# Performance work log

Hardware: AMD Instinct MI355X
Metric: run time of the kernel (lower is better)

The kernel has to match this reference:

```python
import jax, jax.numpy as jnp
import numpy as np
import math

DIM = 64
N_, H_, W_ = 8, 64, 64
EPS = 1e-5


def setup_inputs() -> dict:
    key = jax.random.key(0)
    ks = jax.random.split(key, 11)
    c = DIM
    s = 1.0 / math.sqrt(c)
    x = jax.random.normal(ks[0], (N_, c, H_, W_), dtype=jnp.float32)
    return {
        "x": x,
        "gamma": jnp.ones((c,), jnp.float32),
        "beta": jnp.zeros((c,), jnp.float32),
        "wq": jax.random.normal(ks[1], (c, c), jnp.float32) * s,
        "bq": jax.random.normal(ks[2], (c,), jnp.float32) * 0.01,
        "wk": jax.random.normal(ks[3], (c, c), jnp.float32) * s,
        "bk": jax.random.normal(ks[4], (c,), jnp.float32) * 0.01,
        "wv": jax.random.normal(ks[5], (c, c), jnp.float32) * s,
        "bv": jax.random.normal(ks[6], (c,), jnp.float32) * 0.01,
        "wo": jax.random.normal(ks[7], (c, c), jnp.float32) * s,
        "bo": jax.random.normal(ks[8], (c,), jnp.float32) * 0.01,
    }


def _conv1x1(x, w, b):
    # 1x1 conv == channel mixing: x [n,c,h,w], w [out,in], b [out]
    return jnp.einsum('nchw,oc->nohw', x, w) + b[None, :, None, None]


def _batchnorm(x, gamma, beta):
    # training-mode BatchNorm2d: biased batch stats over (N,H,W)
    mean = jnp.mean(x, axis=(0, 2, 3), keepdims=True)
    var = jnp.var(x, axis=(0, 2, 3), keepdims=True)
    xn = (x - mean) * jax.lax.rsqrt(var + EPS)
    return xn * gamma[None, :, None, None] + beta[None, :, None, None]


def reference(x, gamma, beta, wq, bq, wk, bk, wv, bv, wo, bo):
    n, c, h, w = x.shape
    hw = h * w
    norm_x = _batchnorm(x, gamma, beta)
    q = _conv1x1(norm_x, wq, bq).reshape(n, c, hw)  # [n,c,hw]
    k = _conv1x1(norm_x, wk, bk).reshape(n, c, hw)  # [n,c,hw]
    v = _conv1x1(norm_x, wv, bv).reshape(n, c, hw)  # [n,c,hw]
    # scores [n, hw, hw] = q^T k / sqrt(c) -- full N x N matrix (memory bound)
    scores = jnp.einsum('nci,ncj->nij', q, k) / math.sqrt(c)
    attn = jax.nn.softmax(scores, axis=-1)
    # res [n, hw, c] = attn @ v^T
    res = jnp.einsum('nij,ncj->nic', attn, v)
    # faithful to original: raw reshape [n,hw,c] -> [n,c,h,w] (no transpose)
    res = res.reshape(n, c, h, w)
    res = _conv1x1(res, wo, bo)
    return x + res
```

## Files before the change

kernel.cpp:

```cpp
#include <hip/hip_runtime.h>


#define HW 4096
#define CC 64
#define NBATCH 8
#define SPLIT 4
#define TSTEPS 16
#define QSCALE 0.18033688011112042f

using f32x4 = __attribute__((ext_vector_type(4))) float;
using bf16x8 = __attribute__((ext_vector_type(8))) short;
using u32x2 = __attribute__((ext_vector_type(2))) unsigned int;
typedef unsigned short u16;
typedef unsigned int u32;

#if __has_builtin(__builtin_amdgcn_exp2f)
#define EXP2F(v) __builtin_amdgcn_exp2f(v)
#else
#define EXP2F(v) exp2f(v)
#endif

#define MFMA16(a, b, c) __builtin_amdgcn_mfma_f32_16x16x32_bf16(a, b, c, 0, 0, 0)
#define GLDS(gsrc, ldst)                                              \
  __builtin_amdgcn_global_load_lds(                                   \
      (const __attribute__((address_space(1))) void*)(gsrc),          \
      (__attribute__((address_space(3))) void*)(ldst), 16, 0, 0)

__device__ __forceinline__ u16 f2bf(float v) {
  u32 u = __float_as_uint(v);
  return (u16)((u + 0x7fffu + ((u >> 16) & 1u)) >> 16);
}
__device__ __forceinline__ float bf2f(u16 h) {
  return __uint_as_float(((u32)h) << 16);
}
__device__ __forceinline__ u32 cvtpk_bf16(float lo, float hi) {
  u32 r;
  asm("v_cvt_pk_bf16_f32 %0, %1, %2" : "=v"(r) : "v"(lo), "v"(hi));
  return r;
}

__global__ __launch_bounds__(256) void k_stats1(const float* __restrict__ x,
                                                float* __restrict__ SACC) {
  const int n = blockIdx.x >> 6;
  const int c = blockIdx.x & 63;
  const int tid = threadIdx.x;
  const float* xp = x + ((size_t)n * CC + c) * HW;
  float s1 = 0.f, s2 = 0.f;
#pragma unroll
  for (int i = tid; i < HW; i += 256) {
    const float v = xp[i];
    s1 += v;
    s2 += v * v;
  }
#pragma unroll
  for (int m = 1; m <= 32; m <<= 1) {
    s1 += __shfl_xor(s1, m);
    s2 += __shfl_xor(s2, m);
  }
  __shared__ float r1[4], r2[4];
  const int w = tid >> 6;
  if ((tid & 63) == 0) { r1[w] = s1; r2[w] = s2; }
  __syncthreads();
  if (tid == 0) {
    unsafeAtomicAdd(SACC + c, r1[0] + r1[1] + r1[2] + r1[3]);
    unsafeAtomicAdd(SACC + CC + c, r2[0] + r2[1] + r2[2] + r2[3]);
  }
}

__device__ __forceinline__ void mm16(const float* __restrict__ W,
                                     const float* __restrict__ B,
                                     const float* xcol, int o0, float scale,
                                     float* outv) {
#pragma unroll
  for (int oo = 0; oo < 16; ++oo) {
    const int o = o0 + oo;
    float a = B[o];
#pragma unroll
    for (int c = 0; c < CC; ++c) a = fmaf(W[o * CC + c], xcol[c], a);
    outv[oo] = a * scale;
  }
}

__global__ __launch_bounds__(256) void k_qkv(
    const float* __restrict__ x, const float* __restrict__ SACC,
    const float* __restrict__ gamma, const float* __restrict__ beta,
    const float* __restrict__ wq, const float* __restrict__ bq,
    const float* __restrict__ wk, const float* __restrict__ bk,
    const float* __restrict__ wv, const float* __restrict__ bv,
    u16* __restrict__ QH, u16* __restrict__ QL, u16* __restrict__ KH,
    u16* __restrict__ KL, u16* __restrict__ V) {
  const int n = blockIdx.x >> 6;
  const int i0 = (blockIdx.x & 63) << 6;
  __shared__ float xn[CC][64];
  __shared__ float sa[CC], sb[CC];
  __shared__ u16 TH[64][68];
  __shared__ u16 TL[64][68];
  const int tid = threadIdx.x;
  if (tid < CC) {
    const float inv = 1.0f / (float)(NBATCH * HW);
    const float mean = SACC[tid] * inv;
    const float var = SACC[CC + tid] * inv - mean * mean;
    const float a = rsqrtf(var + 1e-5f) * gamma[tid];
    sa[tid] = a;
    sb[tid] = beta[tid] - mean * a;
  }
  __syncthreads();
  {
    const int p = tid & 63;
    const int c0 = (tid >> 6) << 4;
    const float* xp = x + (size_t)n * CC * HW + i0 + p;
#pragma unroll
    for (int cc = 0; cc < 16; ++cc) {
      const int c = c0 + cc;
      xn[c][p] = fmaf(xp[(size_t)c * HW], sa[c], sb[c]);
    }
  }
  __syncthreads();
  const int w = __builtin_amdgcn_readfirstlane(tid >> 6);
  const int p = tid & 63;
  float xcol[CC];
#pragma unroll
  for (int c = 0; c < CC; ++c) xcol[c] = xn[c][p];

  const size_t rowbase = (size_t)n * HW + i0;
  u32* const th32 = (u32*)&TH[0][0];
  u32* const tl32 = (u32*)&TL[0][0];
  const int wb32 = (p * 68 + w * 16) >> 1;
  const int r = tid >> 2;
  const int q4 = tid & 3;
  const int rb32 = (r * 68 + q4 * 16) >> 1;

  float v16[16];
#pragma unroll
  for (int conv = 0; conv < 2; ++conv) {
    if (conv == 0)
      mm16(wq, bq, xcol, w * 16, QSCALE, v16);
    else
      mm16(wk, bk, xcol, w * 16, 1.0f, v16);
#pragma unroll
    for (int e = 0; e < 8; ++e) {
      const float v0 = v16[2 * e], v1 = v16[2 * e + 1];
      const u16 h0 = f2bf(v0), h1 = f2bf(v1);
      th32[wb32 + e] = (u32)h0 | ((u32)h1 << 16);
      tl32[wb32 + e] =
          (u32)f2bf(v0 - bf2f(h0)) | ((u32)f2bf(v1 - bf2f(h1)) << 16);
    }
    __syncthreads();
    {
      u16* const dh = (conv == 0 ? QH : KH) + (rowbase + r) * CC + q4 * 16;
      u16* const dl = (conv == 0 ? QL : KL) + (rowbase + r) * CC + q4 * 16;
      const u32x2 a0 = *(const u32x2*)&th32[rb32];
      const u32x2 a1 = *(const u32x2*)&th32[rb32 + 2];
      const u32x2 a2 = *(const u32x2*)&th32[rb32 + 4];
      const u32x2 a3 = *(const u32x2*)&th32[rb32 + 6];
      *(uint4*)dh = make_uint4(a0[0], a0[1], a1[0], a1[1]);
      *(uint4*)(dh + 8) = make_uint4(a2[0], a2[1], a3[0], a3[1]);
      const u32x2 b0 = *(const u32x2*)&tl32[rb32];
      const u32x2 b1 = *(const u32x2*)&tl32[rb32 + 2];
      const u32x2 b2 = *(const u32x2*)&tl32[rb32 + 4];
      const u32x2 b3 = *(const u32x2*)&tl32[rb32 + 6];
      *(uint4*)dl = make_uint4(b0[0], b0[1], b1[0], b1[1]);
      *(uint4*)(dl + 8) = make_uint4(b2[0], b2[1], b3[0], b3[1]);
    }
    __syncthreads();
  }
  mm16(wv, bv, xcol, w * 16, 1.0f, v16);
#pragma unroll
  for (int oo = 0; oo < 16; ++oo)
    V[((size_t)n * CC + w * 16 + oo) * HW + i0 + p] = f2bf(v16[oo]);
}

__global__ __launch_bounds__(256, 3) void k_attn(
    const u16* __restrict__ QH, const u16* __restrict__ QL,
    const u16* __restrict__ KH, const u16* __restrict__ KL,
    const u16* __restrict__ V, float* __restrict__ RES,
    float* __restrict__ Z) {
  const int bid = blockIdx.x;
  const int n = bid & 7;
  const int qt = (bid >> 3) & 31;
  const int s = bid >> 8;
  const int tid = threadIdx.x;
  const int w = tid >> 6;
  const int l = tid & 63;
  const int l15 = l & 15;
  const int lg = l >> 4;
  const int qw0 = qt * 128 + w * 32;
  const int key0 = s * (TSTEPS * 64);

  __shared__ alignas(16) u16 KHs[2][64][64];
  __shared__ alignas(16) u16 Vs[2][64][64];
  __shared__ alignas(16) u16 P[4][32][64];

  const int lr8 = l >> 3;
  const u32 eoff = (u32)(((l & 7) * 8) ^ (lr8 << 3));
  const u16* sp[4];
  u16* d0[4];
  u16* d1[4];
  size_t stp[4];
#pragma unroll
  for (int c = 0; c < 4; ++c) {
    const int idx = w * 4 + c;
    const int tile = idx >> 3;
    const int j = idx & 7;
    const int lrow = j * 8 + lr8;
    if (tile == 0) {
      sp[c] = KH + ((size_t)n * HW + key0 + lrow) * CC + eoff;
      stp[c] = (size_t)64 * CC;
      d0[c] = &KHs[0][j * 8][0];
      d1[c] = &KHs[1][j * 8][0];
    } else {
      sp[c] = V + ((size_t)n * CC + lrow) * HW + key0 + eoff;
      stp[c] = 64;
      d0[c] = &Vs[0][j * 8][0];
      d1[c] = &Vs[1][j * 8][0];
    }
  }
  auto stage = [&](int bufsel) {
#pragma unroll
    for (int c = 0; c < 4; ++c) {
      GLDS(sp[c], bufsel ? d1[c] : d0[c]);
      sp[c] += stp[c];
    }
  };

  bf16x8 qh[2][2], ql[2][2];
  {
    const size_t qbase = ((size_t)n * HW + qw0 + l15) * CC + lg * 8;
#pragma unroll
    for (int qb = 0; qb < 2; ++qb)
#pragma unroll
      for (int m = 0; m < 2; ++m) {
        const size_t off = qbase + (size_t)qb * 16 * CC + m * 32;
        qh[qb][m] = *(const bf16x8*)(QH + off);
        ql[qb][m] = *(const bf16x8*)(QL + off);
      }
  }

  f32x4 acc[2][4];
#pragma unroll
  for (int qb = 0; qb < 2; ++qb)
#pragma unroll
    for (int chb = 0; chb < 4; ++chb)
      acc[qb][chb] = (f32x4){0.f, 0.f, 0.f, 0.f};
  float zacc[2] = {0.f, 0.f};

  const u16* klp = KL + ((size_t)n * HW + key0 + l15) * CC + lg * 8;

  stage(0);
  asm volatile("s_waitcnt vmcnt(0)\n\ts_barrier" ::: "memory");

  const int swz = (l15 & 7) << 4;
  char* const Pw = (char*)&P[w][0][0];

#pragma unroll 1
  for (int t = 0; t < TSTEPS; ++t) {
    const int buf = t & 1;
    bf16x8 kl[4][2];
#pragma unroll
    for (int kb = 0; kb < 4; ++kb) {
      kl[kb][0] = *(const bf16x8*)(klp + (size_t)kb * 16 * CC);
      kl[kb][1] = *(const bf16x8*)(klp + (size_t)kb * 16 * CC + 32);
    }
    if (t + 1 < TSTEPS) stage(buf ^ 1);
    const char* khb = (const char*)&KHs[buf][0][0];
    const char* vsb = (const char*)&Vs[buf][0][0];

    f32x4 sc[2][4];
#pragma unroll
    for (int kb = 0; kb < 4; ++kb) {
      const int rb = (kb * 16 + l15) * 128;
      const int c0 = (lg * 16) ^ swz;
      const int c1 = (64 + lg * 16) ^ swz;
      const bf16x8 kh0 = *(const bf16x8*)(khb + rb + c0);
      const bf16x8 kh1 = *(const bf16x8*)(khb + rb + c1);
      __builtin_amdgcn_s_setprio(1);
#pragma unroll
      for (int qb = 0; qb < 2; ++qb) {
        f32x4 s4 = {0.f, 0.f, 0.f, 0.f};
        s4 = MFMA16(kh0, qh[qb][0], s4);
        s4 = MFMA16(kh1, qh[qb][1], s4);
        s4 = MFMA16(kh0, ql[qb][0], s4);
        s4 = MFMA16(kh1, ql[qb][1], s4);
        s4 = MFMA16(kl[kb][0], qh[qb][0], s4);
        s4 = MFMA16(kl[kb][1], qh[qb][1], s4);
        sc[qb][kb] = s4;
      }
      __builtin_amdgcn_s_setprio(0);
    }
#pragma unroll
    for (int qb = 0; qb < 2; ++qb) {
      char* const prow = Pw + (qb * 16 + l15) * 128;
      float zs = 0.f;
#pragma unroll
      for (int kb = 0; kb < 4; ++kb) {
        const float p0 = EXP2F(sc[qb][kb][0]);
        const float p1 = EXP2F(sc[qb][kb][1]);
        const float p2 = EXP2F(sc[qb][kb][2]);
        const float p3 = EXP2F(sc[qb][kb][3]);
        zs += (p0 + p1) + (p2 + p3);
        const u32x2 pk = {cvtpk_bf16(p0, p1), cvtpk_bf16(p2, p3)};
        *(u32x2*)(prow + ((kb * 32 + lg * 8) ^ swz)) = pk;
      }
      zacc[qb] += zs;
    }
#pragma unroll
    for (int m2 = 0; m2 < 2; ++m2) {
      const int cc2 = (m2 * 64 + lg * 16) ^ swz;
      bf16x8 vb[4];
#pragma unroll
      for (int chb = 0; chb < 4; ++chb)
        vb[chb] = *(const bf16x8*)(vsb + (chb * 16 + l15) * 128 + cc2);
      __builtin_amdgcn_s_setprio(1);
#pragma unroll
      for (int qb = 0; qb < 2; ++qb) {
        const bf16x8 pa = *(const bf16x8*)(Pw + (qb * 16 + l15) * 128 + cc2);
#pragma unroll
        for (int chb = 0; chb < 4; ++chb)
          acc[qb][chb] = MFMA16(pa, vb[chb], acc[qb][chb]);
      }
      __builtin_amdgcn_s_setprio(0);
    }
    klp += (size_t)64 * CC;
    asm volatile("s_waitcnt vmcnt(0) lgkmcnt(0)\n\ts_barrier" ::: "memory");
  }

#pragma unroll
  for (int qb = 0; qb < 2; ++qb) {
    zacc[qb] += __shfl_xor(zacc[qb], 16);
    zacc[qb] += __shfl_xor(zacc[qb], 32);
  }
  if (l < 16) {
    unsafeAtomicAdd(Z + (size_t)n * HW + qw0 + l, zacc[0]);
    unsafeAtomicAdd(Z + (size_t)n * HW + qw0 + 16 + l, zacc[1]);
  }
  float* resn = RES + ((size_t)n * HW + qw0) * CC;
#pragma unroll
  for (int qb = 0; qb < 2; ++qb)
#pragma unroll
    for (int r = 0; r < 4; ++r) {
      const int row = qb * 16 + lg * 4 + r;
#pragma unroll
      for (int chb = 0; chb < 4; ++chb)
        unsafeAtomicAdd(resn + (size_t)row * CC + chb * 16 + l15,
                        acc[qb][chb][r]);
    }
}

__global__ __launch_bounds__(256) void k_out(const float* __restrict__ RES,
                                             const float* __restrict__ Z,
                                             const float* __restrict__ x,
                                             const float* __restrict__ wo,
                                             const float* __restrict__ bo,
                                             float* __restrict__ out) {
  const int n = blockIdx.x >> 6;
  const int j = ((blockIdx.x & 63) << 6) + (threadIdx.x & 63);
  const int oq = __builtin_amdgcn_readfirstlane(threadIdx.x >> 6);
  const float* rn = RES + (size_t)n * HW * CC;
  const float* zb = Z + (size_t)n * HW;
  const int jh = j >> 6;
  float rcol[CC];
#pragma unroll
  for (int c2 = 0; c2 < CC; ++c2)
    rcol[c2] = rn[(size_t)c2 * HW + j] * (1.0f / zb[c2 * 64 + jh]);
  const size_t xb = (size_t)n * CC * HW;
  for (int o = oq * 16; o < oq * 16 + 16; ++o) {
    float sacc = bo[o];
#pragma unroll
    for (int c2 = 0; c2 < CC; ++c2)
      sacc = fmaf(wo[o * CC + c2], rcol[c2], sacc);
    out[xb + (size_t)o * HW + j] = x[xb + (size_t)o * HW + j] + sacc;
  }
}

extern "C" void kernel_launch(void* const* d_in, const int* in_sizes, int n_in,
                              void* d_out, int out_size, void* d_ws,
                              size_t ws_size, hipStream_t stream) {
  const float* x = (const float*)d_in[0];
  const float* gamma = (const float*)d_in[1];
  const float* beta = (const float*)d_in[2];
  const float* wq = (const float*)d_in[3];
  const float* bq = (const float*)d_in[4];
  const float* wk = (const float*)d_in[5];
  const float* bk = (const float*)d_in[6];
  const float* wv = (const float*)d_in[7];
  const float* bv = (const float*)d_in[8];
  const float* wo = (const float*)d_in[9];
  const float* bo = (const float*)d_in[10];
  float* out = (float*)d_out;

  char* ws = (char*)d_ws;
  float* SACC = (float*)ws;
  float* Z = (float*)(ws + 1024);
  float* RES = (float*)(ws + 1024 + (size_t)NBATCH * HW * 4);
  const size_t INIT_BYTES =
      1024 + (size_t)NBATCH * HW * 4 + (size_t)NBATCH * HW * CC * 4;
  const size_t ARR = (size_t)NBATCH * HW * CC;
  u16* QH = (u16*)(ws + INIT_BYTES);
  u16* QL = QH + ARR;
  u16* KH = QL + ARR;
  u16* KL = KH + ARR;
  u16* V = KL + ARR;

  hipMemsetAsync(ws, 0, INIT_BYTES, stream);
  hipLaunchKernelGGL(k_stats1, dim3(512), dim3(256), 0, stream, x, SACC);
  hipLaunchKernelGGL(k_qkv, dim3(512), dim3(256), 0, stream, x, SACC, gamma,
                     beta, wq, bq, wk, bk, wv, bv, QH, QL, KH, KL, V);
  hipLaunchKernelGGL(k_attn, dim3(1024), dim3(256), 0, stream, QH, QL, KH, KL,
                     V, RES, Z);
  hipLaunchKernelGGL(k_out, dim3(512), dim3(256), 0, stream, RES, Z, x, wo, bo,
                     out);
}
```

Measured before the change: 272.3 us.

## Prefetch next K-low tile during PV and interleave exp with QK MFMAs

```diff
diff --git a/kernel.cpp b/kernel.cpp
--- a/kernel.cpp
+++ b/kernel.cpp
@@ -25,6 +25,10 @@
   __builtin_amdgcn_global_load_lds(                                   \
       (const __attribute__((address_space(1))) void*)(gsrc),          \
       (__attribute__((address_space(3))) void*)(ldst), 16, 0, 0)
+#define GL16(dst, voff, base, IMM)                                    \
+  asm volatile("global_load_dwordx4 %0, %1, %2 offset:" #IMM          \
+               : "=v"(dst)                                            \
+               : "v"(voff), "s"(base))
 
 __device__ __forceinline__ u16 f2bf(float v) {
   u32 u = __float_as_uint(v);
@@ -244,10 +248,24 @@
       acc[qb][chb] = (f32x4){0.f, 0.f, 0.f, 0.f};
   float zacc[2] = {0.f, 0.f};
 
-  const u16* klp = KL + ((size_t)n * HW + key0 + l15) * CC + lg * 8;
-
+  const u16* klbase = KL + (size_t)n * HW * CC;
+  u32 voff = (u32)(((key0 + l15) * CC + lg * 8) * 2);
+  bf16x8 kl00, kl01, kl10, kl11, kl20, kl21, kl30, kl31;
+  {
+    const u32 voff1 = voff + 4096;
+    GL16(kl00, voff, klbase, 0);
+    GL16(kl01, voff, klbase, 64);
+    GL16(kl10, voff, klbase, 2048);
+    GL16(kl11, voff, klbase, 2112);
+    GL16(kl20, voff1, klbase, 0);
+    GL16(kl21, voff1, klbase, 64);
+    GL16(kl30, voff1, klbase, 2048);
+    GL16(kl31, voff1, klbase, 2112);
+    voff += 64 * CC * 2;
+  }
   stage(0);
   asm volatile("s_waitcnt vmcnt(0)\n\ts_barrier" ::: "memory");
+  __builtin_amdgcn_sched_barrier(0);
 
   const int swz = (l15 & 7) << 4;
   char* const Pw = (char*)&P[w][0][0];
@@ -255,19 +273,14 @@
 #pragma unroll 1
   for (int t = 0; t < TSTEPS; ++t) {
     const int buf = t & 1;
-    bf16x8 kl[4][2];
-#pragma unroll
-    for (int kb = 0; kb < 4; ++kb) {
-      kl[kb][0] = *(const bf16x8*)(klp + (size_t)kb * 16 * CC);
-      kl[kb][1] = *(const bf16x8*)(klp + (size_t)kb * 16 * CC + 32);
-    }
     if (t + 1 < TSTEPS) stage(buf ^ 1);
     const char* khb = (const char*)&KHs[buf][0][0];
     const char* vsb = (const char*)&Vs[buf][0][0];
 
-    f32x4 sc[2][4];
 #pragma unroll
     for (int kb = 0; kb < 4; ++kb) {
+      const bf16x8 klA = (kb == 0) ? kl00 : (kb == 1) ? kl10 : (kb == 2) ? kl20 : kl30;
+      const bf16x8 klB = (kb == 0) ? kl01 : (kb == 1) ? kl11 : (kb == 2) ? kl21 : kl31;
       const int rb = (kb * 16 + l15) * 128;
       const int c0 = (lg * 16) ^ swz;
       const int c1 = (64 + lg * 16) ^ swz;
@@ -281,27 +294,31 @@
         s4 = MFMA16(kh1, qh[qb][1], s4);
         s4 = MFMA16(kh0, ql[qb][0], s4);
         s4 = MFMA16(kh1, ql[qb][1], s4);
-        s4 = MFMA16(kl[kb][0], qh[qb][0], s4);
-        s4 = MFMA16(kl[kb][1], qh[qb][1], s4);
-        sc[qb][kb] = s4;
+        s4 = MFMA16(klA, qh[qb][0], s4);
+        s4 = MFMA16(klB, qh[qb][1], s4);
+        __builtin_amdgcn_s_setprio(0);
+        const float p0 = EXP2F(s4[0]);
+        const float p1 = EXP2F(s4[1]);
+        const float p2 = EXP2F(s4[2]);
+        const float p3 = EXP2F(s4[3]);
+        zacc[qb] += (p0 + p1) + (p2 + p3);
+        const u32x2 pk = {cvtpk_bf16(p0, p1), cvtpk_bf16(p2, p3)};
+        *(u32x2*)(Pw + (qb * 16 + l15) * 128 + ((kb * 32 + lg * 8) ^ swz)) = pk;
+        __builtin_amdgcn_s_setprio(1);
       }
       __builtin_amdgcn_s_setprio(0);
     }
-#pragma unroll
-    for (int qb = 0; qb < 2; ++qb) {
-      char* const prow = Pw + (qb * 16 + l15) * 128;
-      float zs = 0.f;
-#pragma unroll
-      for (int kb = 0; kb < 4; ++kb) {
-        const float p0 = EXP2F(sc[qb][kb][0]);
-        const float p1 = EXP2F(sc[qb][kb][1]);
-        const float p2 = EXP2F(sc[qb][kb][2]);
-        const float p3 = EXP2F(sc[qb][kb][3]);
-        zs += (p0 + p1) + (p2 + p3);
-        const u32x2 pk = {cvtpk_bf16(p0, p1), cvtpk_bf16(p2, p3)};
-        *(u32x2*)(prow + ((kb * 32 + lg * 8) ^ swz)) = pk;
-      }
-      zacc[qb] += zs;
+    {
+      const u32 voff1 = voff + 4096;
+      GL16(kl00, voff, klbase, 0);
+      GL16(kl01, voff, klbase, 64);
+      GL16(kl10, voff, klbase, 2048);
+      GL16(kl11, voff, klbase, 2112);
+      GL16(kl20, voff1, klbase, 0);
+      GL16(kl21, voff1, klbase, 64);
+      GL16(kl30, voff1, klbase, 2048);
+      GL16(kl31, voff1, klbase, 2112);
+      voff += 64 * CC * 2;
     }
 #pragma unroll
     for (int m2 = 0; m2 < 2; ++m2) {
@@ -320,8 +337,8 @@
       }
       __builtin_amdgcn_s_setprio(0);
     }
-    klp += (size_t)64 * CC;
     asm volatile("s_waitcnt vmcnt(0) lgkmcnt(0)\n\ts_barrier" ::: "memory");
+    __builtin_amdgcn_sched_barrier(0);
   }
 
 #pragma unroll
```

New measurement: 274.1 us. Within noise of the previous version (+0.7%).
